# Performance work log

Measured on AMD Instinct MI355X. Metric: run time of the kernel, lower is better.

The kernel has to match this reference:

```python
import jax, jax.numpy as jnp
import numpy as np

LAMBDA_M = 1.0
NUM_GRU_LAYERS = 3

B, S, H, G = 64, 512, 768, 768


def setup_inputs() -> dict:
    key = jax.random.key(0)
    ks = jax.random.split(key, 12)
    std = 0.02
    # variable-length attention mask (all rows non-empty)
    lengths = jax.random.randint(ks[0], (B,), S // 4, S + 1)
    attention_mask = (jnp.arange(S)[None, :] < lengths[:, None]).astype(jnp.float32)
    return {
        "sentence_representation": jax.random.normal(ks[1], (B, H), jnp.float32),
        "attention_mask": attention_mask,
        "aspect_embedding": jax.random.normal(ks[2], (B, H), jnp.float32),
        "sentence_embeddings": jax.random.normal(ks[3], (B, S, H), jnp.float32),
        "ws": std * jax.random.normal(ks[4], (H, H), jnp.float32),
        "wa": std * jax.random.normal(ks[5], (H, H), jnp.float32),
        "w": std * jax.random.normal(ks[6], (H,), jnp.float32),
        "whs": std * jax.random.normal(ks[7], (H, G), jnp.float32),
        "wd1": std * jax.random.normal(ks[8], (H, H), jnp.float32),
        "wd": std * jax.random.normal(ks[9], (G, H), jnp.float32),
        "w_ih": std * jax.random.normal(ks[10], (3 * G, H), jnp.float32),  # GRU input weights (r,z,n)
        "w_hh": std * jax.random.normal(ks[11], (3 * G, G), jnp.float32),  # GRU hidden weights (r,z,n)
    }


def _gru_cell(x, h, w_ih, w_hh):
    # standard GRU cell, bias=False (torch gate order: r, z, n)
    gi = x @ w_ih.T  # (B, 3G)
    gh = h @ w_hh.T  # (B, 3G)
    i_r, i_z, i_n = jnp.split(gi, 3, axis=-1)
    h_r, h_z, h_n = jnp.split(gh, 3, axis=-1)
    r = jax.nn.sigmoid(i_r + h_r)
    z = jax.nn.sigmoid(i_z + h_z)
    n = jnp.tanh(i_n + r * h_n)
    return (1.0 - z) * n + z * h


def reference(sentence_representation, attention_mask, aspect_embedding,
              sentence_embeddings, ws, wa, w, whs, wd1, wd, w_ih, w_hh):
    # Hoist loop-invariant projections (same math as recomputing per layer)
    Se = jnp.einsum('bsh,hk->bsk', sentence_embeddings, ws)  # (B,S,H)
    A = aspect_embedding @ wa                                 # (B,H)
    mask = attention_mask                                     # (B,S)
    denom = mask.sum(-1, keepdims=True)                       # (B,1)
    h = sentence_representation
    for t in range(NUM_GRU_LAYERS):
        Wd = wd1 if t == 0 else wd
        M = Se + (h @ Wd)[:, None, :] + A[:, None, :]         # (B,S,H)
        scores = jnp.tanh(M) @ w                              # (B,S)
        m = jax.nn.softmax(LAMBDA_M * scores, axis=-1)        # (B,S)
        # reweighted masked-mean pooling
        at = jnp.einsum('bs,bsh->bh', m * mask, sentence_embeddings) / denom
        if t == 0:
            h = h @ whs                                       # project to GRU hidden dim
        h = _gru_cell(at, h, w_ih, w_hh)
    return h
```

## Files before the change

kernel.cpp:

```cpp
#include <hip/hip_runtime.h>
#include <hip/hip_bf16.h>
#include <stdint.h>

#define Bdim 64
#define Sdim 512
#define Hdim 768
#define G3   2304

typedef float f32x4 __attribute__((ext_vector_type(4)));
typedef short s16x8 __attribute__((ext_vector_type(8)));
typedef short s16x4 __attribute__((ext_vector_type(4)));

__device__ __forceinline__ float bf2f(unsigned short u){
  union { unsigned int i; float f; } c; c.i = ((unsigned int)u) << 16; return c.f;
}
__device__ __forceinline__ unsigned short f2bf(float f){
  union { float f; unsigned int i; } c; c.f = f;
  unsigned int x = c.i;
  return (unsigned short)((x + 0x7fffu + ((x >> 16) & 1u)) >> 16);
}
__device__ __forceinline__ float fast_tanh(float x){
  float e = __expf(2.f * x);
  return 1.f - 2.f / (e + 1.f);
}
__device__ __forceinline__ float fast_sigmoid(float x){
  return 1.f / (1.f + __expf(-x));
}


__global__ __launch_bounds__(256) void k_conv_bf16(const float* __restrict__ src,
                                                   unsigned short* __restrict__ dst, int n8){
  int i = blockIdx.x * 256 + threadIdx.x;
  if (i >= n8) return;
  const float4* s = (const float4*)src;
  float4 a = s[2*i], b = s[2*i+1];
  uint4 o;
  o.x = (unsigned)f2bf(a.x) | ((unsigned)f2bf(a.y) << 16);
  o.y = (unsigned)f2bf(a.z) | ((unsigned)f2bf(a.w) << 16);
  o.z = (unsigned)f2bf(b.x) | ((unsigned)f2bf(b.y) << 16);
  o.w = (unsigned)f2bf(b.z) | ((unsigned)f2bf(b.w) << 16);
  ((uint4*)dst)[i] = o;
}

__global__ __launch_bounds__(256) void k_conv4(const float* __restrict__ s0, unsigned short* __restrict__ d0, int c0,
                                               const float* __restrict__ s1, unsigned short* __restrict__ d1, int c1,
                                               const float* __restrict__ s2, unsigned short* __restrict__ d2, int c2,
                                               const float* __restrict__ s3, unsigned short* __restrict__ d3, int c3){
  int i = blockIdx.x * 256 + threadIdx.x;
  const float* s; unsigned short* d; int j;
  if (i < c0) { s = s0; d = d0; j = i; }
  else if (i < c0 + c1) { s = s1; d = d1; j = i - c0; }
  else if (i < c0 + c1 + c2) { s = s2; d = d2; j = i - c0 - c1; }
  else if (i < c0 + c1 + c2 + c3) { s = s3; d = d3; j = i - c0 - c1 - c2; }
  else return;
  const float4* sp = (const float4*)s;
  float4 a = sp[2*j], b = sp[2*j+1];
  uint4 o;
  o.x = (unsigned)f2bf(a.x) | ((unsigned)f2bf(a.y) << 16);
  o.y = (unsigned)f2bf(a.z) | ((unsigned)f2bf(a.w) << 16);
  o.z = (unsigned)f2bf(b.x) | ((unsigned)f2bf(b.y) << 16);
  o.w = (unsigned)f2bf(b.z) | ((unsigned)f2bf(b.w) << 16);
  ((uint4*)d)[j] = o;
}

__global__ __launch_bounds__(256) void k_transpose_ws(const float* __restrict__ src,
                                                      unsigned short* __restrict__ dst){
  __shared__ float tile[32][33];
  int bx = blockIdx.x * 32, by = blockIdx.y * 32;
  int tx = threadIdx.x % 32, ty = threadIdx.x / 32;
  for (int j = ty; j < 32; j += 8) tile[j][tx] = src[(size_t)(by + j) * Hdim + bx + tx];
  __syncthreads();
  for (int j = ty; j < 32; j += 8) dst[(size_t)(bx + j) * Hdim + by + tx] = f2bf(tile[tx][j]);
}

__global__ __launch_bounds__(256) void k_transpose4(const float* __restrict__ s0, unsigned short* __restrict__ d0,
                                                    const float* __restrict__ s1, unsigned short* __restrict__ d1,
                                                    const float* __restrict__ s2, unsigned short* __restrict__ d2,
                                                    const float* __restrict__ s3, unsigned short* __restrict__ d3){
  const float* src; unsigned short* dst;
  switch (blockIdx.z) {
    case 0: src = s0; dst = d0; break;
    case 1: src = s1; dst = d1; break;
    case 2: src = s2; dst = d2; break;
    default: src = s3; dst = d3; break;
  }
  __shared__ float tile[32][33];
  int bx = blockIdx.x * 32, by = blockIdx.y * 32;
  int tx = threadIdx.x % 32, ty = threadIdx.x / 32;
  for (int j = ty; j < 32; j += 8) tile[j][tx] = src[(size_t)(by + j) * Hdim + bx + tx];
  __syncthreads();
  for (int j = ty; j < 32; j += 8) dst[(size_t)(bx + j) * Hdim + by + tx] = f2bf(tile[tx][j]);
}

__global__ __launch_bounds__(256) void k_gemm_se(const unsigned short* __restrict__ A,
                                                 const unsigned short* __restrict__ Bt,
                                                 unsigned short* __restrict__ C){
  __shared__ unsigned short As[128 * 64];
  __shared__ unsigned short Bs[128 * 64];
  const int t = threadIdx.x;
  const int lane = t & 63;
  const int w = t >> 6, wr = w >> 1, wc = w & 1;
  int bid = blockIdx.x;
  int swz = (bid & 7) * 192 + (bid >> 3);
  const int m0 = (swz / 6) * 128, n0 = (swz % 6) * 128;

  f32x4 acc[4][4];
  #pragma unroll
  for (int m = 0; m < 4; m++)
    #pragma unroll
    for (int n = 0; n < 4; n++) acc[m][n] = (f32x4){0.f, 0.f, 0.f, 0.f};

  for (int k0 = 0; k0 < Hdim; k0 += 64) {
    #pragma unroll
    for (int i = 0; i < 4; i++) {
      int L = t * 16 + i * 4096;
      int row = L >> 7;
      int off = L & 127;
      int soff = off ^ ((row & 7) << 4);
      uint4 va = *(const uint4*)((const char*)A  + ((size_t)(m0 + row) * Hdim + k0) * 2 + off);
      uint4 vb = *(const uint4*)((const char*)Bt + ((size_t)(n0 + row) * Hdim + k0) * 2 + off);
      *(uint4*)((char*)As + row * 128 + soff) = va;
      *(uint4*)((char*)Bs + row * 128 + soff) = vb;
    }
    __syncthreads();
    #pragma unroll
    for (int kk = 0; kk < 2; kk++) {
      s16x8 af[4], bfr[4];
      #pragma unroll
      for (int m = 0; m < 4; m++) {
        int row = wr * 64 + m * 16 + (lane & 15);
        int sw = (row & 7) << 4;
        int kb = kk * 64 + (lane >> 4) * 8;
        s16x4 lo = *(const s16x4*)((const char*)As + row * 128 + (kb ^ sw));
        s16x4 hi = *(const s16x4*)((const char*)As + row * 128 + ((kb + 32) ^ sw));
        af[m] = __builtin_shufflevector(lo, hi, 0, 1, 2, 3, 4, 5, 6, 7);
      }
      #pragma unroll
      for (int n = 0; n < 4; n++) {
        int row = wc * 64 + n * 16 + (lane & 15);
        int sw = (row & 7) << 4;
        int kb = kk * 64 + (lane >> 4) * 8;
        s16x4 lo = *(const s16x4*)((const char*)Bs + row * 128 + (kb ^ sw));
        s16x4 hi = *(const s16x4*)((const char*)Bs + row * 128 + ((kb + 32) ^ sw));
        bfr[n] = __builtin_shufflevector(lo, hi, 0, 1, 2, 3, 4, 5, 6, 7);
      }
      #pragma unroll
      for (int m = 0; m < 4; m++)
        #pragma unroll
        for (int n = 0; n < 4; n++)
          acc[m][n] = __builtin_amdgcn_mfma_f32_16x16x32_bf16(af[m], bfr[n], acc[m][n], 0, 0, 0);
    }
    __syncthreads();
  }
  #pragma unroll
  for (int m = 0; m < 4; m++) {
    int rowb = m0 + wr * 64 + m * 16 + (lane >> 4) * 4;
    #pragma unroll
    for (int n = 0; n < 4; n++) {
      int col = n0 + wc * 64 + n * 16 + (lane & 15);
      #pragma unroll
      for (int r = 0; r < 4; r++)
        C[(size_t)(rowb + r) * Hdim + col] = f2bf(acc[m][n][r]);
    }
  }
}

__global__ __launch_bounds__(256) void k_gemm_smallM(const unsigned short* __restrict__ A,
                                                     const unsigned short* __restrict__ Bt,
                                                     float* __restrict__ C,
                                                     unsigned short* __restrict__ Cb){
  __shared__ unsigned short As[64 * 64];
  __shared__ unsigned short Bs[128 * 64];
  const int t = threadIdx.x, lane = t & 63, w = t >> 6;
  const int n0 = blockIdx.x * 128;
  f32x4 acc[4][2];
  #pragma unroll
  for (int m = 0; m < 4; m++)
    #pragma unroll
    for (int n = 0; n < 2; n++) acc[m][n] = (f32x4){0.f, 0.f, 0.f, 0.f};

  for (int k0 = 0; k0 < Hdim; k0 += 64) {
    #pragma unroll
    for (int i = 0; i < 2; i++) {
      int L = t * 16 + i * 4096, row = L >> 7, off = L & 127;
      *(uint4*)((char*)As + row * 128 + (off ^ ((row & 7) << 4))) =
        *(const uint4*)((const char*)A + ((size_t)row * Hdim + k0) * 2 + off);
    }
    #pragma unroll
    for (int i = 0; i < 4; i++) {
      int L = t * 16 + i * 4096, row = L >> 7, off = L & 127;
      *(uint4*)((char*)Bs + row * 128 + (off ^ ((row & 7) << 4))) =
        *(const uint4*)((const char*)Bt + ((size_t)(n0 + row) * Hdim + k0) * 2 + off);
    }
    __syncthreads();
    #pragma unroll
    for (int kk = 0; kk < 2; kk++) {
      s16x8 af[4], bfr[2];
      int kb = kk * 64 + (lane >> 4) * 8;
      #pragma unroll
      for (int m = 0; m < 4; m++) {
        int row = m * 16 + (lane & 15);
        int sw = (row & 7) << 4;
        s16x4 lo = *(const s16x4*)((const char*)As + row * 128 + (kb ^ sw));
        s16x4 hi = *(const s16x4*)((const char*)As + row * 128 + ((kb + 32) ^ sw));
        af[m] = __builtin_shufflevector(lo, hi, 0, 1, 2, 3, 4, 5, 6, 7);
      }
      #pragma unroll
      for (int n = 0; n < 2; n++) {
        int row = w * 32 + n * 16 + (lane & 15);
        int sw = (row & 7) << 4;
        s16x4 lo = *(const s16x4*)((const char*)Bs + row * 128 + (kb ^ sw));
        s16x4 hi = *(const s16x4*)((const char*)Bs + row * 128 + ((kb + 32) ^ sw));
        bfr[n] = __builtin_shufflevector(lo, hi, 0, 1, 2, 3, 4, 5, 6, 7);
      }
      #pragma unroll
      for (int m = 0; m < 4; m++)
        #pragma unroll
        for (int n = 0; n < 2; n++)
          acc[m][n] = __builtin_amdgcn_mfma_f32_16x16x32_bf16(af[m], bfr[n], acc[m][n], 0, 0, 0);
    }
    __syncthreads();
  }
  #pragma unroll
  for (int m = 0; m < 4; m++) {
    int rowb = m * 16 + (lane >> 4) * 4;
    #pragma unroll
    for (int n = 0; n < 2; n++) {
      int col = n0 + w * 32 + n * 16 + (lane & 15);
      #pragma unroll
      for (int r = 0; r < 4; r++) {
        float v = acc[m][n][r];
        C[(size_t)(rowb + r) * Hdim + col] = v;
        if (Cb) Cb[(size_t)(rowb + r) * Hdim + col] = f2bf(v);
      }
    }
  }
}

__global__ __launch_bounds__(256) void k_vpart(const unsigned short* __restrict__ A1,
                                               const unsigned short* __restrict__ B1t,
                                               const unsigned short* __restrict__ A2,
                                               const unsigned short* __restrict__ B2t,
                                               float* __restrict__ Vp){
  __shared__ unsigned short As[64 * 64];
  __shared__ unsigned short Bs[128 * 64];
  const int t = threadIdx.x, lane = t & 63, w = t >> 6;
  const int n0 = blockIdx.x * 128;
  const int kc = blockIdx.y;
  f32x4 acc[4][2];
  #pragma unroll
  for (int m = 0; m < 4; m++)
    #pragma unroll
    for (int n = 0; n < 2; n++) acc[m][n] = (f32x4){0.f, 0.f, 0.f, 0.f};

  #pragma unroll
  for (int gi = 0; gi < 4; gi++) {
    int g = kc * 4 + gi;
    const unsigned short* A  = (g < 12) ? A1 : A2;
    const unsigned short* Bt = (g < 12) ? B1t : B2t;
    int k0 = (g % 12) * 64;
    #pragma unroll
    for (int i = 0; i < 2; i++) {
      int L = t * 16 + i * 4096, row = L >> 7, off = L & 127;
      *(uint4*)((char*)As + row * 128 + (off ^ ((row & 7) << 4))) =
        *(const uint4*)((const char*)A + ((size_t)row * Hdim + k0) * 2 + off);
    }
    #pragma unroll
    for (int i = 0; i < 4; i++) {
      int L = t * 16 + i * 4096, row = L >> 7, off = L & 127;
      *(uint4*)((char*)Bs + row * 128 + (off ^ ((row & 7) << 4))) =
        *(const uint4*)((const char*)Bt + ((size_t)(n0 + row) * Hdim + k0) * 2 + off);
    }
    __syncthreads();
    #pragma unroll
    for (int kk = 0; kk < 2; kk++) {
      s16x8 af[4], bfr[2];
      int kb = kk * 64 + (lane >> 4) * 8;
      #pragma unroll
      for (int m = 0; m < 4; m++) {
        int row = m * 16 + (lane & 15);
        int sw = (row & 7) << 4;
        s16x4 lo = *(const s16x4*)((const char*)As + row * 128 + (kb ^ sw));
        s16x4 hi = *(const s16x4*)((const char*)As + row * 128 + ((kb + 32) ^ sw));
        af[m] = __builtin_shufflevector(lo, hi, 0, 1, 2, 3, 4, 5, 6, 7);
      }
      #pragma unroll
      for (int n = 0; n < 2; n++) {
        int row = w * 32 + n * 16 + (lane & 15);
        int sw = (row & 7) << 4;
        s16x4 lo = *(const s16x4*)((const char*)Bs + row * 128 + (kb ^ sw));
        s16x4 hi = *(const s16x4*)((const char*)Bs + row * 128 + ((kb + 32) ^ sw));
        bfr[n] = __builtin_shufflevector(lo, hi, 0, 1, 2, 3, 4, 5, 6, 7);
      }
      #pragma unroll
      for (int m = 0; m < 4; m++)
        #pragma unroll
        for (int n = 0; n < 2; n++)
          acc[m][n] = __builtin_amdgcn_mfma_f32_16x16x32_bf16(af[m], bfr[n], acc[m][n], 0, 0, 0);
    }
    __syncthreads();
  }
  float* outp = Vp + (size_t)kc * (Bdim * Hdim);
  #pragma unroll
  for (int m = 0; m < 4; m++) {
    int rowb = m * 16 + (lane >> 4) * 4;
    #pragma unroll
    for (int n = 0; n < 2; n++) {
      int col = n0 + w * 32 + n * 16 + (lane & 15);
      #pragma unroll
      for (int r = 0; r < 4; r++)
        outp[(size_t)(rowb + r) * Hdim + col] = acc[m][n][r];
    }
  }
}

__global__ __launch_bounds__(256) void k_scores(const unsigned short* __restrict__ Seb,
                                                const float* __restrict__ Vp,
                                                const float* __restrict__ wv,
                                                float* __restrict__ scores){
  int b = blockIdx.y;
  int s_base = blockIdx.x * 16;
  int t = threadIdx.x, lane = t & 63, w = t >> 6;
  f32x4 v0 = {0,0,0,0}, v1 = {0,0,0,0}, v2 = {0,0,0,0};
  #pragma unroll
  for (int kc = 0; kc < 6; kc++) {
    const float* Vb = Vp + ((size_t)kc * Bdim + b) * Hdim;
    v0 += *(const f32x4*)(Vb + lane * 8);
    v1 += *(const f32x4*)(Vb + lane * 8 + 4);
    v2 += *(const f32x4*)(Vb + 512 + lane * 4);
  }
  f32x4 w0 = *(const f32x4*)(wv + lane * 8);
  f32x4 w1 = *(const f32x4*)(wv + lane * 8 + 4);
  f32x4 w2 = *(const f32x4*)(wv + 512 + lane * 4);
  #pragma unroll
  for (int si = 0; si < 4; si++) {
    int s = s_base + w * 4 + si;
    const unsigned short* rp = Seb + ((size_t)b * Sdim + s) * Hdim;
    ushort4 p0 = *(const ushort4*)(rp + lane * 8);
    ushort4 p1 = *(const ushort4*)(rp + lane * 8 + 4);
    ushort4 p2 = *(const ushort4*)(rp + 512 + lane * 4);
    float acc;
    acc  = fast_tanh(bf2f(p0.x) + v0[0]) * w0[0];
    acc += fast_tanh(bf2f(p0.y) + v0[1]) * w0[1];
    acc += fast_tanh(bf2f(p0.z) + v0[2]) * w0[2];
    acc += fast_tanh(bf2f(p0.w) + v0[3]) * w0[3];
    acc += fast_tanh(bf2f(p1.x) + v1[0]) * w1[0];
    acc += fast_tanh(bf2f(p1.y) + v1[1]) * w1[1];
    acc += fast_tanh(bf2f(p1.z) + v1[2]) * w1[2];
    acc += fast_tanh(bf2f(p1.w) + v1[3]) * w1[3];
    acc += fast_tanh(bf2f(p2.x) + v2[0]) * w2[0];
    acc += fast_tanh(bf2f(p2.y) + v2[1]) * w2[1];
    acc += fast_tanh(bf2f(p2.z) + v2[2]) * w2[2];
    acc += fast_tanh(bf2f(p2.w) + v2[3]) * w2[3];
    #pragma unroll
    for (int o = 32; o; o >>= 1) acc += __shfl_xor(acc, o);
    if (lane == 0) scores[(size_t)b * Sdim + s] = acc;
  }
}

__global__ __launch_bounds__(512) void k_softmax(const float* __restrict__ scores,
                                                 const float* __restrict__ mask,
                                                 float* __restrict__ mwn){
  int b = blockIdx.x, t = threadIdx.x, lane = t & 63, w = t >> 6;
  __shared__ float r1[8], r2[8];
  float x = scores[(size_t)b * Sdim + t];
  float mk = mask[(size_t)b * Sdim + t];
  float mx = x;
  #pragma unroll
  for (int o = 32; o; o >>= 1) mx = fmaxf(mx, __shfl_xor(mx, o));
  if (lane == 0) r1[w] = mx;
  __syncthreads();
  mx = r1[0];
  #pragma unroll
  for (int i = 1; i < 8; i++) mx = fmaxf(mx, r1[i]);
  __syncthreads();
  float e = __expf(x - mx);
  float se = e, sm = mk;
  #pragma unroll
  for (int o = 32; o; o >>= 1) { se += __shfl_xor(se, o); sm += __shfl_xor(sm, o); }
  if (lane == 0) { r1[w] = se; r2[w] = sm; }
  __syncthreads();
  se = 0.f; sm = 0.f;
  #pragma unroll
  for (int i = 0; i < 8; i++) { se += r1[i]; sm += r2[i]; }
  mwn[(size_t)b * Sdim + t] = (e / se) * mk / sm;
}

__global__ __launch_bounds__(192) void k_at_part_bf16(const unsigned short* __restrict__ SEb,
                                                      const float* __restrict__ mwn,
                                                      float* __restrict__ at_part){
  int sc = blockIdx.x, b = blockIdx.y;
  int t = threadIdx.x;
  __shared__ float msh[64];
  __shared__ float half0[96 * 8];
  if (t < 64) msh[t] = mwn[(size_t)b * Sdim + sc * 64 + t];
  __syncthreads();
  int hseg = t % 96, sh = t / 96;
  const unsigned short* base = SEb + ((size_t)b * Sdim + sc * 64 + sh * 32) * Hdim + hseg * 8;
  float acc[8] = {0, 0, 0, 0, 0, 0, 0, 0};
  for (int s = 0; s < 32; s++) {
    float m = msh[sh * 32 + s];
    ushort4 a = *(const ushort4*)(base + (size_t)s * Hdim);
    ushort4 c = *(const ushort4*)(base + (size_t)s * Hdim + 4);
    acc[0] += m * bf2f(a.x); acc[1] += m * bf2f(a.y); acc[2] += m * bf2f(a.z); acc[3] += m * bf2f(a.w);
    acc[4] += m * bf2f(c.x); acc[5] += m * bf2f(c.y); acc[6] += m * bf2f(c.z); acc[7] += m * bf2f(c.w);
  }
  if (sh == 0) {
    #pragma unroll
    for (int j = 0; j < 8; j++) half0[hseg * 8 + j] = acc[j];
  }
  __syncthreads();
  if (sh == 1) {
    float* op = at_part + ((size_t)sc * Bdim + b) * Hdim + hseg * 8;
    #pragma unroll
    for (int j = 0; j < 8; j++) op[j] = acc[j] + half0[hseg * 8 + j];
  }
}

__global__ __launch_bounds__(192) void k_at_part_f32(const float* __restrict__ SE,
                                                     const float* __restrict__ mwn,
                                                     float* __restrict__ at_part){
  int sc = blockIdx.x, b = blockIdx.y;
  int t = threadIdx.x;
  __shared__ float msh[64];
  __shared__ float half0[96 * 8];
  if (t < 64) msh[t] = mwn[(size_t)b * Sdim + sc * 64 + t];
  __syncthreads();
  int hseg = t % 96, sh = t / 96;
  const float* base = SE + ((size_t)b * Sdim + sc * 64 + sh * 32) * Hdim + hseg * 8;
  float acc[8] = {0, 0, 0, 0, 0, 0, 0, 0};
  for (int s = 0; s < 32; s++) {
    float m = msh[sh * 32 + s];
    float4 a = *(const float4*)(base + (size_t)s * Hdim);
    float4 c = *(const float4*)(base + (size_t)s * Hdim + 4);
    acc[0] += m * a.x; acc[1] += m * a.y; acc[2] += m * a.z; acc[3] += m * a.w;
    acc[4] += m * c.x; acc[5] += m * c.y; acc[6] += m * c.z; acc[7] += m * c.w;
  }
  if (sh == 0) {
    #pragma unroll
    for (int j = 0; j < 8; j++) half0[hseg * 8 + j] = acc[j];
  }
  __syncthreads();
  if (sh == 1) {
    float* op = at_part + ((size_t)sc * Bdim + b) * Hdim + hseg * 8;
    #pragma unroll
    for (int j = 0; j < 8; j++) op[j] = acc[j] + half0[hseg * 8 + j];
  }
}

__global__ __launch_bounds__(256) void k_at_reduce(const float* __restrict__ at_part,
                                                   unsigned short* __restrict__ atb){
  int i = blockIdx.x * 256 + threadIdx.x;
  float s = 0.f;
  #pragma unroll
  for (int p = 0; p < 8; p++) s += at_part[(size_t)p * (Bdim * Hdim) + i];
  atb[i] = f2bf(s);
}

__global__ __launch_bounds__(256) void k_gates2(const unsigned short* __restrict__ atb,
                                                const unsigned short* __restrict__ hb,
                                                const unsigned short* __restrict__ w_ihb,
                                                const unsigned short* __restrict__ w_hhb,
                                                float* __restrict__ gi2,
                                                float* __restrict__ gh2){
  __shared__ unsigned short As[64 * 64];
  __shared__ unsigned short Bs[128 * 64];
  const int t = threadIdx.x, lane = t & 63, w = t >> 6;
  const int n0 = blockIdx.x * 128;
  const int z = blockIdx.y, kc = blockIdx.z;
  const unsigned short* A  = z ? hb : atb;
  const unsigned short* Bt = z ? w_hhb : w_ihb;
  float* outp = (z ? gh2 : gi2) + (size_t)kc * (Bdim * G3);
  f32x4 acc[4][2];
  #pragma unroll
  for (int m = 0; m < 4; m++)
    #pragma unroll
    for (int n = 0; n < 2; n++) acc[m][n] = (f32x4){0.f, 0.f, 0.f, 0.f};

  for (int it = 0; it < 6; it++) {
    int k0 = kc * 384 + it * 64;
    #pragma unroll
    for (int i = 0; i < 2; i++) {
      int L = t * 16 + i * 4096, row = L >> 7, off = L & 127;
      *(uint4*)((char*)As + row * 128 + (off ^ ((row & 7) << 4))) =
        *(const uint4*)((const char*)A + ((size_t)row * Hdim + k0) * 2 + off);
    }
    #pragma unroll
    for (int i = 0; i < 4; i++) {
      int L = t * 16 + i * 4096, row = L >> 7, off = L & 127;
      *(uint4*)((char*)Bs + row * 128 + (off ^ ((row & 7) << 4))) =
        *(const uint4*)((const char*)Bt + ((size_t)(n0 + row) * Hdim + k0) * 2 + off);
    }
    __syncthreads();
    #pragma unroll
    for (int kk = 0; kk < 2; kk++) {
      s16x8 af[4], bfr[2];
      int kb = kk * 64 + (lane >> 4) * 8;
      #pragma unroll
      for (int m = 0; m < 4; m++) {
        int row = m * 16 + (lane & 15);
        int sw = (row & 7) << 4;
        s16x4 lo = *(const s16x4*)((const char*)As + row * 128 + (kb ^ sw));
        s16x4 hi = *(const s16x4*)((const char*)As + row * 128 + ((kb + 32) ^ sw));
        af[m] = __builtin_shufflevector(lo, hi, 0, 1, 2, 3, 4, 5, 6, 7);
      }
      #pragma unroll
      for (int n = 0; n < 2; n++) {
        int row = w * 32 + n * 16 + (lane & 15);
        int sw = (row & 7) << 4;
        s16x4 lo = *(const s16x4*)((const char*)Bs + row * 128 + (kb ^ sw));
        s16x4 hi = *(const s16x4*)((const char*)Bs + row * 128 + ((kb + 32) ^ sw));
        bfr[n] = __builtin_shufflevector(lo, hi, 0, 1, 2, 3, 4, 5, 6, 7);
      }
      #pragma unroll
      for (int m = 0; m < 4; m++)
        #pragma unroll
        for (int n = 0; n < 2; n++)
          acc[m][n] = __builtin_amdgcn_mfma_f32_16x16x32_bf16(af[m], bfr[n], acc[m][n], 0, 0, 0);
    }
    __syncthreads();
  }
  #pragma unroll
  for (int m = 0; m < 4; m++) {
    int rowb = m * 16 + (lane >> 4) * 4;
    #pragma unroll
    for (int n = 0; n < 2; n++) {
      int col = n0 + w * 32 + n * 16 + (lane & 15);
      #pragma unroll
      for (int r = 0; r < 4; r++)
        outp[(size_t)(rowb + r) * G3 + col] = acc[m][n][r];
    }
  }
}

__global__ __launch_bounds__(256) void k_gru_elem2(const float* __restrict__ gi2,
                                                   const float* __restrict__ gh2,
                                                   const float* __restrict__ h,
                                                   float* __restrict__ hout,
                                                   unsigned short* __restrict__ hbout){
  int i = blockIdx.x * 256 + threadIdx.x;
  int b = i / Hdim, g = i % Hdim;
  const size_t P = (size_t)Bdim * G3;
  const float* gia = gi2 + (size_t)b * G3;
  const float* gha = gh2 + (size_t)b * G3;
  float ir = gia[g] + gia[P + g];
  float iz = gia[Hdim + g] + gia[P + Hdim + g];
  float in_ = gia[2 * Hdim + g] + gia[P + 2 * Hdim + g];
  float hr = gha[g] + gha[P + g];
  float hz = gha[Hdim + g] + gha[P + Hdim + g];
  float hn = gha[2 * Hdim + g] + gha[P + 2 * Hdim + g];
  float r = fast_sigmoid(ir + hr);
  float z = fast_sigmoid(iz + hz);
  float n = fast_tanh(in_ + r * hn);
  float ho = (1.f - z) * n + z * h[i];
  hout[i] = ho;
  hbout[i] = f2bf(ho);
}

extern "C" void kernel_launch(void* const* d_in, const int* in_sizes, int n_in,
                              void* d_out, int out_size, void* d_ws, size_t ws_size,
                              hipStream_t stream) {
  const float* sr   = (const float*)d_in[0];
  const float* mask = (const float*)d_in[1];
  const float* asp  = (const float*)d_in[2];
  const float* SE   = (const float*)d_in[3];
  const float* ws_  = (const float*)d_in[4];
  const float* wa   = (const float*)d_in[5];
  const float* wv   = (const float*)d_in[6];
  const float* whs  = (const float*)d_in[7];
  const float* wd1  = (const float*)d_in[8];
  const float* wd   = (const float*)d_in[9];
  const float* w_ih = (const float*)d_in[10];
  const float* w_hh = (const float*)d_in[11];
  float* out = (float*)d_out;

  char* p = (char*)d_ws;
  size_t offA = 0;
  auto A_ = [&](size_t b) -> char* { char* r = p + offA; offA += b; return r; };
  unsigned short* Seb  = (unsigned short*)A_(50331648);
  unsigned short* wsbT = (unsigned short*)A_(1179648);
  unsigned short* SEb  = (unsigned short*)A_(50331648);

  const size_t othersBytes = 18100224;
  bool keepSEb = (offA + othersBytes) <= ws_size;
  char* q = keepSEb ? (p + offA) : (char*)SEb;
  size_t o2 = 0;
  auto B_ = [&](size_t b) -> char* { char* r = q + o2; o2 += b; return r; };
  unsigned short* w_ihb = (unsigned short*)B_(3538944);
  unsigned short* w_hhb = (unsigned short*)B_(3538944);
  unsigned short* wd1T  = (unsigned short*)B_(1179648);
  unsigned short* wdT   = (unsigned short*)B_(1179648);
  unsigned short* waT   = (unsigned short*)B_(1179648);
  unsigned short* whsT  = (unsigned short*)B_(1179648);
  unsigned short* srb   = (unsigned short*)B_(98304);
  unsigned short* aspb  = (unsigned short*)B_(98304);
  float* Vp      = (float*)B_(1179648);
  float* scores  = (float*)B_(131072);
  float* mwn     = (float*)B_(131072);
  float* at_part = (float*)B_(1572864);
  unsigned short* atb = (unsigned short*)B_(98304);
  float* gi2     = (float*)B_(1179648);
  float* gh2     = (float*)B_(1179648);
  float* hA      = (float*)B_(196608);
  float* hB      = (float*)B_(196608);
  unsigned short* hbA = (unsigned short*)B_(98304);
  unsigned short* hbB = (unsigned short*)B_(98304);
  if (!keepSEb && (offA > ws_size)) return;

  k_conv_bf16<<<dim3(12288), dim3(256), 0, stream>>>(SE, SEb, 3145728);
  k_transpose_ws<<<dim3(24, 24), dim3(256), 0, stream>>>(ws_, wsbT);
  k_gemm_se<<<dim3(1536), dim3(256), 0, stream>>>(SEb, wsbT, Seb);
  k_transpose4<<<dim3(24, 24, 4), dim3(256), 0, stream>>>(wd1, wd1T, wd, wdT, wa, waT, whs, whsT);
  k_conv4<<<dim3(1776), dim3(256), 0, stream>>>(w_ih, w_ihb, 221184, w_hh, w_hhb, 221184,
                                                sr, srb, 6144, asp, aspb, 6144);
  k_gemm_smallM<<<dim3(6), dim3(256), 0, stream>>>(srb, whsT, hA, hbA);
  k_vpart<<<dim3(6, 6), dim3(256), 0, stream>>>(srb, wd1T, aspb, waT, Vp);

  const unsigned short* SEb_pool = keepSEb ? SEb : nullptr;
  const float* hcur = hA;
  const unsigned short* hbcur = hbA;
  for (int tl = 0; tl < 3; ++tl) {
    if (tl > 0)
      k_vpart<<<dim3(6, 6), dim3(256), 0, stream>>>(hbcur, wdT, aspb, waT, Vp);
    k_scores<<<dim3(32, 64), dim3(256), 0, stream>>>(Seb, Vp, wv, scores);
    k_softmax<<<dim3(64), dim3(512), 0, stream>>>(scores, mask, mwn);
    if (keepSEb)
      k_at_part_bf16<<<dim3(8, 64), dim3(192), 0, stream>>>(SEb_pool, mwn, at_part);
    else
      k_at_part_f32<<<dim3(8, 64), dim3(192), 0, stream>>>(SE, mwn, at_part);
    k_at_reduce<<<dim3(192), dim3(256), 0, stream>>>(at_part, atb);
    k_gates2<<<dim3(18, 2, 2), dim3(256), 0, stream>>>(atb, hbcur, w_ihb, w_hhb, gi2, gh2);
    float* hout = (tl == 2) ? out : ((hcur == hA) ? hB : hA);
    unsigned short* hbout = (hbcur == hbA) ? hbB : hbA;
    k_gru_elem2<<<dim3(192), dim3(256), 0, stream>>>(gi2, gh2, hcur, hout, hbout);
    hcur = hout;
    hbcur = hbout;
  }
}
```

Before: 263.4 us.

## Merge prep kernels, fuse softmax into pooling, use direct global-to-LDS loads in GEMM

All preprocessing (SE bf16 conversion, weight transposes, weight and vector conversions) is merged into one launch. The per-layer softmax kernel is folded into the pooling kernel, with each block recomputing the row softmax redundantly. The SE GEMM now stages tiles with global_load_lds instead of register round-trips, pre-swizzling the global address so the LDS layout stays the same. This cuts launch count and intermediate traffic, at the cost of redundant softmax work per block and a GEMM staging path that relies on the readfirstlane wave-uniform base being correct.

```diff
diff --git a/kernel.cpp b/kernel.cpp
--- a/kernel.cpp
+++ b/kernel.cpp
@@ -26,7 +26,56 @@
 __device__ __forceinline__ float fast_sigmoid(float x){
   return 1.f / (1.f + __expf(-x));
 }
-
+__device__ __forceinline__ void gload16(const void* g, void* l){
+  __builtin_amdgcn_global_load_lds((const __attribute__((address_space(1))) void*)g,
+                                   (__attribute__((address_space(3))) void*)l, 16, 0, 0);
+}
+
+__global__ __launch_bounds__(256) void k_prep(const float* __restrict__ SE, unsigned short* __restrict__ SEb,
+                                              const float* __restrict__ ws_, unsigned short* __restrict__ wsbT,
+                                              const float* __restrict__ wd1, unsigned short* __restrict__ wd1T,
+                                              const float* __restrict__ wd,  unsigned short* __restrict__ wdT,
+                                              const float* __restrict__ wa,  unsigned short* __restrict__ waT,
+                                              const float* __restrict__ whs, unsigned short* __restrict__ whsT,
+                                              const float* __restrict__ w_ih, unsigned short* __restrict__ w_ihb,
+                                              const float* __restrict__ w_hh, unsigned short* __restrict__ w_hhb,
+                                              const float* __restrict__ sr,  unsigned short* __restrict__ srb,
+                                              const float* __restrict__ asp, unsigned short* __restrict__ aspb){
+  __shared__ float tile[32][33];
+  int bid = blockIdx.x;
+  if (bid < 2880) {
+    int which = bid / 576, r = bid % 576;
+    const float* src; unsigned short* dst;
+    switch (which) {
+      case 0: src = ws_; dst = wsbT; break;
+      case 1: src = wd1; dst = wd1T; break;
+      case 2: src = wd;  dst = wdT;  break;
+      case 3: src = wa;  dst = waT;  break;
+      default: src = whs; dst = whsT; break;
+    }
+    int bx = (r % 24) * 32, by = (r / 24) * 32;
+    int tx = threadIdx.x % 32, ty = threadIdx.x / 32;
+    for (int j = ty; j < 32; j += 8) tile[j][tx] = src[(size_t)(by + j) * Hdim + bx + tx];
+    __syncthreads();
+    for (int j = ty; j < 32; j += 8) dst[(size_t)(bx + j) * Hdim + by + tx] = f2bf(tile[tx][j]);
+    return;
+  }
+  bid -= 2880;
+  const float* s; unsigned short* d; int j;
+  if      (bid < 12288) { s = SE;   d = SEb;   j = bid * 256 + threadIdx.x; }
+  else if (bid < 13152) { s = w_ih; d = w_ihb; j = (bid - 12288) * 256 + threadIdx.x; }
+  else if (bid < 14016) { s = w_hh; d = w_hhb; j = (bid - 13152) * 256 + threadIdx.x; }
+  else if (bid < 14040) { s = sr;   d = srb;   j = (bid - 14016) * 256 + threadIdx.x; }
+  else                  { s = asp;  d = aspb;  j = (bid - 14040) * 256 + threadIdx.x; }
+  const float4* sp = (const float4*)s;
+  float4 a = sp[2*j], b = sp[2*j+1];
+  uint4 o;
+  o.x = (unsigned)f2bf(a.x) | ((unsigned)f2bf(a.y) << 16);
+  o.y = (unsigned)f2bf(a.z) | ((unsigned)f2bf(a.w) << 16);
+  o.z = (unsigned)f2bf(b.x) | ((unsigned)f2bf(b.y) << 16);
+  o.w = (unsigned)f2bf(b.z) | ((unsigned)f2bf(b.w) << 16);
+  ((uint4*)d)[j] = o;
+}
 
 __global__ __launch_bounds__(256) void k_conv_bf16(const float* __restrict__ src,
                                                    unsigned short* __restrict__ dst, int n8){
@@ -115,12 +164,11 @@
     for (int i = 0; i < 4; i++) {
       int L = t * 16 + i * 4096;
       int row = L >> 7;
-      int off = L & 127;
-      int soff = off ^ ((row & 7) << 4);
-      uint4 va = *(const uint4*)((const char*)A  + ((size_t)(m0 + row) * Hdim + k0) * 2 + off);
-      uint4 vb = *(const uint4*)((const char*)Bt + ((size_t)(n0 + row) * Hdim + k0) * 2 + off);
-      *(uint4*)((char*)As + row * 128 + soff) = va;
-      *(uint4*)((char*)Bs + row * 128 + soff) = vb;
+      int offp = L & 127;
+      int goff = offp ^ ((row & 7) << 4);
+      int wub = __builtin_amdgcn_readfirstlane((t & 192) * 16 + i * 4096);
+      gload16((const char*)A  + ((size_t)(m0 + row) * Hdim + k0) * 2 + goff, (char*)As + wub);
+      gload16((const char*)Bt + ((size_t)(n0 + row) * Hdim + k0) * 2 + goff, (char*)Bs + wub);
     }
     __syncthreads();
     #pragma unroll
@@ -358,42 +406,50 @@
   }
 }
 
-__global__ __launch_bounds__(512) void k_softmax(const float* __restrict__ scores,
-                                                 const float* __restrict__ mask,
-                                                 float* __restrict__ mwn){
-  int b = blockIdx.x, t = threadIdx.x, lane = t & 63, w = t >> 6;
-  __shared__ float r1[8], r2[8];
-  float x = scores[(size_t)b * Sdim + t];
-  float mk = mask[(size_t)b * Sdim + t];
-  float mx = x;
-  #pragma unroll
-  for (int o = 32; o; o >>= 1) mx = fmaxf(mx, __shfl_xor(mx, o));
-  if (lane == 0) r1[w] = mx;
-  __syncthreads();
-  mx = r1[0];
-  #pragma unroll
-  for (int i = 1; i < 8; i++) mx = fmaxf(mx, r1[i]);
-  __syncthreads();
-  float e = __expf(x - mx);
-  float se = e, sm = mk;
-  #pragma unroll
-  for (int o = 32; o; o >>= 1) { se += __shfl_xor(se, o); sm += __shfl_xor(sm, o); }
-  if (lane == 0) { r1[w] = se; r2[w] = sm; }
-  __syncthreads();
-  se = 0.f; sm = 0.f;
-  #pragma unroll
-  for (int i = 0; i < 8; i++) { se += r1[i]; sm += r2[i]; }
-  mwn[(size_t)b * Sdim + t] = (e / se) * mk / sm;
-}
-
-__global__ __launch_bounds__(192) void k_at_part_bf16(const unsigned short* __restrict__ SEb,
-                                                      const float* __restrict__ mwn,
-                                                      float* __restrict__ at_part){
+__global__ __launch_bounds__(192) void k_at_sm_bf16(const unsigned short* __restrict__ SEb,
+                                                    const float* __restrict__ scores,
+                                                    const float* __restrict__ mask,
+                                                    float* __restrict__ at_part){
   int sc = blockIdx.x, b = blockIdx.y;
-  int t = threadIdx.x;
+  int t = threadIdx.x, lane = t & 63, w = t >> 6;
+  __shared__ float sbuf[512];
+  __shared__ float mbuf[512];
+  __shared__ float red[3], red2[3];
   __shared__ float msh[64];
   __shared__ float half0[96 * 8];
-  if (t < 64) msh[t] = mwn[(size_t)b * Sdim + sc * 64 + t];
+  float lmax = -1e30f;
+  #pragma unroll
+  for (int j = 0; j < 3; j++) {
+    int idx = t + 192 * j;
+    if (idx < 512) {
+      float v = scores[(size_t)b * Sdim + idx];
+      float mk = mask[(size_t)b * Sdim + idx];
+      sbuf[idx] = v; mbuf[idx] = mk;
+      lmax = fmaxf(lmax, v);
+    }
+  }
+  #pragma unroll
+  for (int o = 32; o; o >>= 1) lmax = fmaxf(lmax, __shfl_xor(lmax, o));
+  if (lane == 0) red[w] = lmax;
+  __syncthreads();
+  float mx = fmaxf(fmaxf(red[0], red[1]), red[2]);
+  float le = 0.f, lm = 0.f;
+  #pragma unroll
+  for (int j = 0; j < 3; j++) {
+    int idx = t + 192 * j;
+    if (idx < 512) {
+      float e = __expf(sbuf[idx] - mx);
+      le += e; lm += mbuf[idx];
+      sbuf[idx] = e * mbuf[idx];
+    }
+  }
+  #pragma unroll
+  for (int o = 32; o; o >>= 1) { le += __shfl_xor(le, o); lm += __shfl_xor(lm, o); }
+  __syncthreads();
+  if (lane == 0) { red[w] = le; red2[w] = lm; }
+  __syncthreads();
+  float inv = 1.f / ((red[0] + red[1] + red[2]) * (red2[0] + red2[1] + red2[2]));
+  if (t < 64) msh[t] = sbuf[sc * 64 + t] * inv;
   __syncthreads();
   int hseg = t % 96, sh = t / 96;
   const unsigned short* base = SEb + ((size_t)b * Sdim + sc * 64 + sh * 32) * Hdim + hseg * 8;
@@ -417,14 +473,50 @@
   }
 }
 
-__global__ __launch_bounds__(192) void k_at_part_f32(const float* __restrict__ SE,
-                                                     const float* __restrict__ mwn,
-                                                     float* __restrict__ at_part){
+__global__ __launch_bounds__(192) void k_at_sm_f32(const float* __restrict__ SE,
+                                                   const float* __restrict__ scores,
+                                                   const float* __restrict__ mask,
+                                                   float* __restrict__ at_part){
   int sc = blockIdx.x, b = blockIdx.y;
-  int t = threadIdx.x;
+  int t = threadIdx.x, lane = t & 63, w = t >> 6;
+  __shared__ float sbuf[512];
+  __shared__ float mbuf[512];
+  __shared__ float red[3], red2[3];
   __shared__ float msh[64];
   __shared__ float half0[96 * 8];
-  if (t < 64) msh[t] = mwn[(size_t)b * Sdim + sc * 64 + t];
+  float lmax = -1e30f;
+  #pragma unroll
+  for (int j = 0; j < 3; j++) {
+    int idx = t + 192 * j;
+    if (idx < 512) {
+      float v = scores[(size_t)b * Sdim + idx];
+      float mk = mask[(size_t)b * Sdim + idx];
+      sbuf[idx] = v; mbuf[idx] = mk;
+      lmax = fmaxf(lmax, v);
+    }
+  }
+  #pragma unroll
+  for (int o = 32; o; o >>= 1) lmax = fmaxf(lmax, __shfl_xor(lmax, o));
+  if (lane == 0) red[w] = lmax;
+  __syncthreads();
+  float mx = fmaxf(fmaxf(red[0], red[1]), red[2]);
+  float le = 0.f, lm = 0.f;
+  #pragma unroll
+  for (int j = 0; j < 3; j++) {
+    int idx = t + 192 * j;
+    if (idx < 512) {
+      float e = __expf(sbuf[idx] - mx);
+      le += e; lm += mbuf[idx];
+      sbuf[idx] = e * mbuf[idx];
+    }
+  }
+  #pragma unroll
+  for (int o = 32; o; o >>= 1) { le += __shfl_xor(le, o); lm += __shfl_xor(lm, o); }
+  __syncthreads();
+  if (lane == 0) { red[w] = le; red2[w] = lm; }
+  __syncthreads();
+  float inv = 1.f / ((red[0] + red[1] + red[2]) * (red2[0] + red2[1] + red2[2]));
+  if (t < 64) msh[t] = sbuf[sc * 64 + t] * inv;
   __syncthreads();
   int hseg = t % 96, sh = t / 96;
   const float* base = SE + ((size_t)b * Sdim + sc * 64 + sh * 32) * Hdim + hseg * 8;
@@ -596,7 +688,6 @@
   unsigned short* aspb  = (unsigned short*)B_(98304);
   float* Vp      = (float*)B_(1179648);
   float* scores  = (float*)B_(131072);
-  float* mwn     = (float*)B_(131072);
   float* at_part = (float*)B_(1572864);
   unsigned short* atb = (unsigned short*)B_(98304);
   float* gi2     = (float*)B_(1179648);
@@ -607,27 +698,32 @@
   unsigned short* hbB = (unsigned short*)B_(98304);
   if (!keepSEb && (offA > ws_size)) return;
 
-  k_conv_bf16<<<dim3(12288), dim3(256), 0, stream>>>(SE, SEb, 3145728);
-  k_transpose_ws<<<dim3(24, 24), dim3(256), 0, stream>>>(ws_, wsbT);
-  k_gemm_se<<<dim3(1536), dim3(256), 0, stream>>>(SEb, wsbT, Seb);
-  k_transpose4<<<dim3(24, 24, 4), dim3(256), 0, stream>>>(wd1, wd1T, wd, wdT, wa, waT, whs, whsT);
-  k_conv4<<<dim3(1776), dim3(256), 0, stream>>>(w_ih, w_ihb, 221184, w_hh, w_hhb, 221184,
-                                                sr, srb, 6144, asp, aspb, 6144);
+  if (keepSEb) {
+    k_prep<<<dim3(16944), dim3(256), 0, stream>>>(SE, SEb, ws_, wsbT, wd1, wd1T, wd, wdT,
+                                                  wa, waT, whs, whsT, w_ih, w_ihb, w_hh, w_hhb,
+                                                  sr, srb, asp, aspb);
+    k_gemm_se<<<dim3(1536), dim3(256), 0, stream>>>(SEb, wsbT, Seb);
+  } else {
+    k_conv_bf16<<<dim3(12288), dim3(256), 0, stream>>>(SE, SEb, 3145728);
+    k_transpose_ws<<<dim3(24, 24), dim3(256), 0, stream>>>(ws_, wsbT);
+    k_gemm_se<<<dim3(1536), dim3(256), 0, stream>>>(SEb, wsbT, Seb);
+    k_transpose4<<<dim3(24, 24, 4), dim3(256), 0, stream>>>(wd1, wd1T, wd, wdT, wa, waT, whs, whsT);
+    k_conv4<<<dim3(1776), dim3(256), 0, stream>>>(w_ih, w_ihb, 221184, w_hh, w_hhb, 221184,
+                                                  sr, srb, 6144, asp, aspb, 6144);
+  }
   k_gemm_smallM<<<dim3(6), dim3(256), 0, stream>>>(srb, whsT, hA, hbA);
   k_vpart<<<dim3(6, 6), dim3(256), 0, stream>>>(srb, wd1T, aspb, waT, Vp);
 
-  const unsigned short* SEb_pool = keepSEb ? SEb : nullptr;
   const float* hcur = hA;
   const unsigned short* hbcur = hbA;
   for (int tl = 0; tl < 3; ++tl) {
     if (tl > 0)
       k_vpart<<<dim3(6, 6), dim3(256), 0, stream>>>(hbcur, wdT, aspb, waT, Vp);
     k_scores<<<dim3(32, 64), dim3(256), 0, stream>>>(Seb, Vp, wv, scores);
-    k_softmax<<<dim3(64), dim3(512), 0, stream>>>(scores, mask, mwn);
     if (keepSEb)
-      k_at_part_bf16<<<dim3(8, 64), dim3(192), 0, stream>>>(SEb_pool, mwn, at_part);
+      k_at_sm_bf16<<<dim3(8, 64), dim3(192), 0, stream>>>(SEb, scores, mask, at_part);
     else
-      k_at_part_f32<<<dim3(8, 64), dim3(192), 0, stream>>>(SE, mwn, at_part);
+      k_at_sm_f32<<<dim3(8, 64), dim3(192), 0, stream>>>(SE, scores, mask, at_part);
     k_at_reduce<<<dim3(192), dim3(256), 0, stream>>>(at_part, atb);
     k_gates2<<<dim3(18, 2, 2), dim3(256), 0, stream>>>(atb, hbcur, w_ihb, w_hhb, gi2, gh2);
     float* hout = (tl == 2) ? out : ((hcur == hA) ? hB : hA);
```

Result: faster. 241.9 us (-8.2%).
